# Kernel optimization log

Hardware: AMD Instinct MI355X
Metric: run time of the kernel (lower is better)

Reference implementation:

```python
import jax, jax.numpy as jnp
import numpy as np

NL, D, H, DFF = 6, 1024, 16, 4096
HD = D // H


def _rope(x):
    # x: [B, L, H, HD]; rotate-half RoPE applied along seq dim 1
    L = x.shape[1]
    half = HD // 2
    inv = 1.0 / (10000.0 ** (jnp.arange(half, dtype=jnp.float32) / half))
    ang = jnp.arange(L, dtype=jnp.float32)[:, None] * inv  # [L, half]
    cos = jnp.cos(ang)[None, :, None, :]
    sin = jnp.sin(ang)[None, :, None, :]
    x1, x2 = x[..., :half], x[..., half:]
    return jnp.concatenate([x1 * cos - x2 * sin, x1 * sin + x2 * cos], axis=-1)


def _ln(x, eps=1e-5):
    m = jnp.mean(x, axis=-1, keepdims=True)
    v = jnp.var(x, axis=-1, keepdims=True)
    return (x - m) * jax.lax.rsqrt(v + eps)


def _adaln(x, emb, w, b):
    # emb: [B,1,D] -> squeeze; proj -> gamma,beta
    gb = emb[:, 0, :] @ w.T + b  # [B, 2D]
    g, be = jnp.split(gb, 2, axis=-1)
    return _ln(x) * (1.0 + g[:, None, :]) + be[:, None, :]


def _attn(q, k, v, mask):
    # q:[B,Lq,H,HD] k,v:[B,Lkv,H,HD] mask:[B,Lkv] True=ignore
    scores = jnp.einsum('bqhd,bkhd->bhqk', q, k) / np.float32(np.sqrt(HD))
    scores = jnp.where(mask[:, None, None, :], jnp.float32(-jnp.inf), scores)
    w = jax.nn.softmax(scores, axis=-1)
    return jnp.einsum('bhqk,bkhd->bqhd', w, v)


def setup_inputs() -> dict:
    key = jax.random.key(0)
    ks = jax.random.split(key, 20)
    B, L, LC = 4, 1024, 512
    s = 0.02
    inp = {
        'x': jax.random.normal(ks[0], (B, L, D), jnp.float32),
        'noise_emb': jax.random.normal(ks[1], (B, 1, D), jnp.float32),
        'context': jax.random.normal(ks[2], (B, LC, D), jnp.float32),
        'src_mask': jnp.zeros((B, L), bool),
        'ctx_mask': jnp.zeros((B, LC), bool),
        'n1_w': jax.random.normal(ks[3], (NL, 2 * D, D), jnp.float32) * s,
        'n1_b': jnp.zeros((NL, 2 * D), jnp.float32),
        'n2_w': jax.random.normal(ks[4], (NL, 2 * D, D), jnp.float32) * s,
        'n2_b': jnp.zeros((NL, 2 * D), jnp.float32),
        'n3_w': jax.random.normal(ks[5], (NL, 2 * D, D), jnp.float32) * s,
        'n3_b': jnp.zeros((NL, 2 * D), jnp.float32),
        'qkv_w': jax.random.normal(ks[6], (NL, 3 * D, D), jnp.float32) * s,
        'so_w': jax.random.normal(ks[7], (NL, D, D), jnp.float32) * s,
        'cq_w': jax.random.normal(ks[8], (NL, D, D), jnp.float32) * s,
        'ck_w': jax.random.normal(ks[9], (NL, D, D), jnp.float32) * s,
        'cv_w': jax.random.normal(ks[10], (NL, D, D), jnp.float32) * s,
        'co_w': jax.random.normal(ks[11], (NL, D, D), jnp.float32) * s,
        'f1_w': jax.random.normal(ks[12], (NL, DFF, D), jnp.float32) * s,
        'f1_b': jnp.zeros((NL, DFF), jnp.float32),
        'f2_w': jax.random.normal(ks[13], (NL, D, DFF), jnp.float32) * s,
        'f2_b': jnp.zeros((NL, D), jnp.float32),
    }
    return inp


def reference(x, noise_emb, context, src_mask, ctx_mask,
              n1_w, n1_b, n2_w, n2_b, n3_w, n3_b,
              qkv_w, so_w, cq_w, ck_w, cv_w, co_w,
              f1_w, f1_b, f2_w, f2_b):
    B, L, _ = x.shape
    LC = context.shape[1]
    for i in range(NL):
        # self-attention with AdaLN pre-norm
        xn = _adaln(x, noise_emb, n1_w[i], n1_b[i])
        qkv = xn @ qkv_w[i].T  # [B,L,3D]
        q, k, v = jnp.split(qkv, 3, axis=-1)
        q = _rope(q.reshape(B, L, H, HD))
        k = _rope(k.reshape(B, L, H, HD))
        v = v.reshape(B, L, H, HD)
        a = _attn(q, k, v, src_mask).reshape(B, L, D) @ so_w[i].T
        x = x + a
        # cross-attention with AdaLN pre-norm
        xn = _adaln(x, noise_emb, n2_w[i], n2_b[i])
        q = _rope((xn @ cq_w[i].T).reshape(B, L, H, HD))
        k = _rope((context @ ck_w[i].T).reshape(B, LC, H, HD))
        v = (context @ cv_w[i].T).reshape(B, LC, H, HD)
        a = _attn(q, k, v, ctx_mask).reshape(B, L, D) @ co_w[i].T
        x = x + a
        # FFN with AdaLN pre-norm
        xn = _adaln(x, noise_emb, n3_w[i], n3_b[i])
        h = jax.nn.gelu(xn @ f1_w[i].T + f1_b[i], approximate=False)
        x = x + (h @ f2_w[i].T + f2_b[i])
    return x
```

## Files before the change

### kernel.cpp

```cpp
#include <hip/hip_runtime.h>
#include <hip/hip_bf16.h>
#include <math.h>

#define D_    1024
#define H_    16
#define HD_   64
#define NL_   6
#define DFF_  4096
#define B_    4
#define L_    1024
#define LC_   512

typedef short bf16x8 __attribute__((ext_vector_type(8)));
typedef float f32x4  __attribute__((ext_vector_type(4)));
typedef unsigned int uint32;

__device__ __forceinline__ float waveReduceSum(float v) {
#pragma unroll
  for (int off = 32; off > 0; off >>= 1) v += __shfl_xor(v, off);
  return v;
}
__device__ __forceinline__ ushort f2bf(float f) {
  union { __hip_bfloat16 h; ushort u; } c;
  c.h = __float2bfloat16(f);
  return c.u;
}
__device__ __forceinline__ float bf2f(ushort u) {
  union { uint32 i; float f; } c;
  c.i = ((uint32)u) << 16;
  return c.f;
}
__device__ __forceinline__ uint32 pk2(float a, float b) {
  return (uint32)f2bf(a) | ((uint32)f2bf(b) << 16);
}
__device__ __forceinline__ void gload16(const ushort* g, ushort* l) {
  __builtin_amdgcn_global_load_lds(
      (const __attribute__((address_space(1))) uint32*)g,
      (__attribute__((address_space(3))) uint32*)l, 16, 0, 0);
}

__global__ __launch_bounds__(256) void cvt_bf16_kernel(
    const float* __restrict__ in, ushort* __restrict__ out, int n4) {
  int i = blockIdx.x * 256 + threadIdx.x;
  int stride = gridDim.x * 256;
  for (; i < n4; i += stride) {
    float4 v = ((const float4*)in)[i];
    ushort4 o = {f2bf(v.x), f2bf(v.y), f2bf(v.z), f2bf(v.w)};
    ((ushort4*)out)[i] = o;
  }
}

__global__ __launch_bounds__(256) void cvt_pack_kv_kernel(
    const float* __restrict__ ck, const float* __restrict__ cv,
    ushort* __restrict__ out, int n4) {
  int i = blockIdx.x * 256 + threadIdx.x;
  int stride = gridDim.x * 256;
  for (; i < n4; i += stride) {
    int row = i >> 8;
    int cb = i & 255;
    int layer = row >> 11;
    int sel = (row >> 10) & 1;
    int r = row & 1023;
    const float* src = (sel ? cv : ck) +
                       (((size_t)layer << 10) + r) * 1024 + cb * 4;
    float4 v = *(const float4*)src;
    ushort4 o = {f2bf(v.x), f2bf(v.y), f2bf(v.z), f2bf(v.w)};
    ((ushort4*)out)[i] = o;
  }
}

__global__ void rope_table_kernel(float* __restrict__ tab) {
  int t = blockIdx.x * 256 + threadIdx.x;
  if (t >= L_ * 32) return;
  int l = t >> 5, j = t & 31;
  float inv = powf(10000.f, -(float)j * (1.f / 32.f));
  float ang = (float)l * inv;
  tab[l * 64 + j] = cosf(ang);
  tab[l * 64 + 32 + j] = sinf(ang);
}

__global__ __launch_bounds__(256) void adaln_gb_all_kernel(
    const float* __restrict__ emb,
    const float* __restrict__ n1w, const float* __restrict__ n2w,
    const float* __restrict__ n3w,
    const float* __restrict__ n1b, const float* __restrict__ n2b,
    const float* __restrict__ n3b,
    float* __restrict__ gb) {
  int wid = blockIdx.x * 4 + (threadIdx.x >> 6);
  int lane = threadIdx.x & 63;
  int n = wid & 2047;
  int g = wid >> 11;
  int layer = g / 3, j = g - layer * 3;
  const float* wbase = (j == 0 ? n1w : (j == 1 ? n2w : n3w));
  const float* bbase = (j == 0 ? n1b : (j == 1 ? n2b : n3b));
  const float* wr = wbase + ((size_t)layer * 2048 + n) * 1024;
  float s0 = 0.f, s1 = 0.f, s2 = 0.f, s3 = 0.f;
#pragma unroll
  for (int k4 = 0; k4 < 4; ++k4) {
    int idx = k4 * 64 + lane;
    float4 w4 = ((const float4*)wr)[idx];
    float4 e0 = ((const float4*)emb)[idx];
    float4 e1 = ((const float4*)(emb + 1024))[idx];
    float4 e2 = ((const float4*)(emb + 2048))[idx];
    float4 e3 = ((const float4*)(emb + 3072))[idx];
    s0 += w4.x * e0.x + w4.y * e0.y + w4.z * e0.z + w4.w * e0.w;
    s1 += w4.x * e1.x + w4.y * e1.y + w4.z * e1.z + w4.w * e1.w;
    s2 += w4.x * e2.x + w4.y * e2.y + w4.z * e2.z + w4.w * e2.w;
    s3 += w4.x * e3.x + w4.y * e3.y + w4.z * e3.z + w4.w * e3.w;
  }
  s0 = waveReduceSum(s0);
  s1 = waveReduceSum(s1);
  s2 = waveReduceSum(s2);
  s3 = waveReduceSum(s3);
  if (lane == 0) {
    float bb = bbase[(size_t)layer * 2048 + n];
    gb[((size_t)g * 4 + 0) * 2048 + n] = s0 + bb;
    gb[((size_t)g * 4 + 1) * 2048 + n] = s1 + bb;
    gb[((size_t)g * 4 + 2) * 2048 + n] = s2 + bb;
    gb[((size_t)g * 4 + 3) * 2048 + n] = s3 + bb;
  }
}

__global__ __launch_bounds__(256) void adaln_apply_kernel(
    const float* __restrict__ x, const float* __restrict__ gb,
    ushort* __restrict__ xn) {
  int r = blockIdx.x;
  int b = r >> 10;
  const float* xr = x + (size_t)r * D_;
  int tid = threadIdx.x;
  float4 v = *(const float4*)(xr + tid * 4);
  float s = v.x + v.y + v.z + v.w;
  float q = v.x * v.x + v.y * v.y + v.z * v.z + v.w * v.w;
  s = waveReduceSum(s);
  q = waveReduceSum(q);
  __shared__ float ssum[4], ssq[4], stats[2];
  int w = tid >> 6, lane = tid & 63;
  if (lane == 0) { ssum[w] = s; ssq[w] = q; }
  __syncthreads();
  if (tid == 0) {
    float S = ssum[0] + ssum[1] + ssum[2] + ssum[3];
    float Q = ssq[0] + ssq[1] + ssq[2] + ssq[3];
    float mean = S * (1.f / D_);
    float var = Q * (1.f / D_) - mean * mean;
    stats[0] = mean;
    stats[1] = rsqrtf(var + 1e-5f);
  }
  __syncthreads();
  float mean = stats[0], rstd = stats[1];
  const float* gp = gb + (size_t)b * 2048;
  float4 g  = *(const float4*)(gp + tid * 4);
  float4 be = *(const float4*)(gp + D_ + tid * 4);
  ushort4 o;
  o.x = f2bf((v.x - mean) * rstd * (1.f + g.x) + be.x);
  o.y = f2bf((v.y - mean) * rstd * (1.f + g.y) + be.y);
  o.z = f2bf((v.z - mean) * rstd * (1.f + g.z) + be.z);
  o.w = f2bf((v.w - mean) * rstd * (1.f + g.w) + be.w);
  *(ushort4*)(xn + (size_t)r * D_ + tid * 4) = o;
}

template <int FLAGS, bool OUTBF, int ROPE>
__global__ __launch_bounds__(256) void gemm_mfma_kernel(
    const ushort* __restrict__ A, int lda,
    const ushort* __restrict__ W, int ldw,
    const float* __restrict__ bias,
    const float* __restrict__ res, int ldres,
    void* __restrict__ Cout, int ldc, int K,
    const float* __restrict__ tab, int rlim, int lmask) {
  __shared__ __align__(16) ushort lds[24576];
  const int tid = threadIdx.x;
  const int lane = tid & 63, wv = tid >> 6;
  const int wrow = (wv >> 1) * 64, wcol = (wv & 1) * 64;
  const int fr = lane & 15;
  const int kbs = (((lane >> 4) ^ (fr & 3)) & 3) * 8;

  const int nwg = gridDim.x * gridDim.y;
  const int wg = blockIdx.y * gridDim.x + blockIdx.x;
  const int q = nwg >> 3;
  const int swz = (wg & 7) * q + (wg >> 3);
  const int row0 = (swz / gridDim.x) * 128;
  const int col0 = (swz % gridDim.x) * 128;

  const int c0 = wv * 2, c1 = wv * 2 + 1;
  const int sr = lane >> 2;
  const int sc = (((lane & 3) ^ (sr & 3)) & 3) * 8;
  const ushort* Ap0 = A + (size_t)(row0 + c0 * 16 + sr) * lda + sc;
  const ushort* Ap1 = A + (size_t)(row0 + c1 * 16 + sr) * lda + sc;
  const ushort* Wp0 = W + (size_t)(col0 + c0 * 16 + sr) * ldw + sc;
  const ushort* Wp1 = W + (size_t)(col0 + c1 * 16 + sr) * ldw + sc;

  f32x4 acc[4][4];
#pragma unroll
  for (int m = 0; m < 4; ++m)
#pragma unroll
    for (int n = 0; n < 4; ++n) acc[m][n] = (f32x4)0.f;

#define ASB(B) (lds + (B) * 4096)
#define WSB(B) (lds + 12288 + (B) * 4096)
#define STAGE(B, T)                                   \
  do {                                                \
    const int koff_ = (T) * 32;                       \
    gload16(Ap0 + koff_, ASB(B) + c0 * 512);          \
    gload16(Ap1 + koff_, ASB(B) + c1 * 512);          \
    gload16(Wp0 + koff_, WSB(B) + c0 * 512);          \
    gload16(Wp1 + koff_, WSB(B) + c1 * 512);          \
  } while (0)
#define WAITV8() asm volatile("s_waitcnt vmcnt(8)" ::: "memory")
#define WAITV4() asm volatile("s_waitcnt vmcnt(4)" ::: "memory")
#define WAITV0() asm volatile("s_waitcnt vmcnt(0)" ::: "memory")
#define BAR()    __builtin_amdgcn_s_barrier()
#define COMPUTE(B)                                                          \
  do {                                                                      \
    bf16x8 af[4], bfr[4];                                                   \
    _Pragma("unroll")                                                       \
    for (int m = 0; m < 4; ++m)                                             \
      af[m] = *(const bf16x8*)(ASB(B) + (wrow + m * 16 + fr) * 32 + kbs);   \
    _Pragma("unroll")                                                       \
    for (int n = 0; n < 4; ++n)                                             \
      bfr[n] = *(const bf16x8*)(WSB(B) + (wcol + n * 16 + fr) * 32 + kbs);  \
    _Pragma("unroll")                                                       \
    for (int m = 0; m < 4; ++m)                                             \
      _Pragma("unroll")                                                     \
      for (int n = 0; n < 4; ++n)                                           \
        acc[m][n] = __builtin_amdgcn_mfma_f32_16x16x32_bf16(af[m], bfr[n],  \
                                                            acc[m][n], 0, 0, 0); \
  } while (0)

  const int NT = K >> 5;
  STAGE(0, 0);
  STAGE(1, 1);
  for (int t = 0; t < NT; t += 3) {
    {
      const bool sA = (t + 2) < NT;
      if (sA) STAGE(2, t + 2);
      if ((t + 1) < NT) { if (sA) WAITV8(); else WAITV4(); } else WAITV0();
      BAR(); COMPUTE(0); BAR();
    }
    if ((t + 1) < NT) {
      const bool sB = (t + 3) < NT;
      if (sB) STAGE(0, t + 3);
      if ((t + 2) < NT) { if (sB) WAITV8(); else WAITV4(); } else WAITV0();
      BAR(); COMPUTE(1); BAR();
    }
    if ((t + 2) < NT) {
      const bool sC = (t + 4) < NT;
      if (sC) STAGE(1, t + 4);
      if ((t + 3) < NT) { if (sC) WAITV8(); else WAITV4(); } else WAITV0();
      BAR(); COMPUTE(2); BAR();
    }
  }
#undef STAGE
#undef WAITV8
#undef WAITV4
#undef WAITV0
#undef COMPUTE

  float bn[4];
  if (FLAGS & 1) {
#pragma unroll
    for (int n = 0; n < 4; ++n) bn[n] = bias[col0 + wcol + n * 16 + fr];
  }
#define EPI(v, n)                                                     \
  do {                                                                \
    if (FLAGS & 1) (v) += bn[n];                                      \
    if (FLAGS & 2) (v) = 0.5f * (v) * (1.f + erff((v) * 0.70710678118f)); \
  } while (0)

  if (OUTBF) {
    ushort* Ct = lds;
    ushort* Cg = (ushort*)Cout;
#pragma unroll
    for (int m = 0; m < 4; ++m) {
      int lr0 = wrow + m * 16 + (lane >> 4) * 4;
#pragma unroll
      for (int n = 0; n < 4; ++n) {
        int lc = wcol + n * 16 + fr;
#pragma unroll
        for (int r = 0; r < 4; ++r) {
          float v = acc[m][n][r];
          EPI(v, n);
          Ct[(lr0 + r) * 136 + lc] = f2bf(v);
        }
      }
    }
    __syncthreads();
#pragma unroll
    for (int it = 0; it < 8; ++it) {
      int lr = (tid >> 4) + it * 16;
      int lc = (tid & 15) * 8;
      union { int4 v; ushort us[8]; } vv;
      vv.v = *(const int4*)&Ct[lr * 136 + lc];
      if (ROPE && (col0 + lc) < rlim) {
        union { int4 v; ushort us[8]; } pv;
        pv.v = *(const int4*)&Ct[lr * 136 + (lc ^ 32)];
        int l = (row0 + lr) & lmask;
        int j = lc & 31;
        const float* cb = &tab[l * 64 + j];
        bool lowhalf = (lc & 63) < 32;
#pragma unroll
        for (int e = 0; e < 8; ++e) {
          float cc = cb[e], ss = cb[32 + e];
          float xv = bf2f(vv.us[e]), xp = bf2f(pv.us[e]);
          float o = lowhalf ? (xv * cc - xp * ss) : (xp * ss + xv * cc);
          vv.us[e] = f2bf(o);
        }
      }
      *(int4*)&Cg[(size_t)(row0 + lr) * ldc + col0 + lc] = vv.v;
    }
  } else {
    float* Cf = (float*)lds;
    float* Cg = (float*)Cout;
#pragma unroll
    for (int half = 0; half < 2; ++half) {
      if ((wv >> 1) == half) {
#pragma unroll
        for (int m = 0; m < 4; ++m) {
          int lr0 = m * 16 + (lane >> 4) * 4;
#pragma unroll
          for (int n = 0; n < 4; ++n) {
            int lc = wcol + n * 16 + fr;
#pragma unroll
            for (int r = 0; r < 4; ++r) {
              float v = acc[m][n][r];
              EPI(v, n);
              Cf[(lr0 + r) * 132 + lc] = v;
            }
          }
        }
      }
      __syncthreads();
#pragma unroll
      for (int it = 0; it < 8; ++it) {
        int lr = (tid >> 5) + it * 8;
        int lc = (tid & 31) * 4;
        int grow = row0 + half * 64 + lr;
        float4 v = *(const float4*)&Cf[lr * 132 + lc];
        if (FLAGS & 4) {
          float4 rv = *(const float4*)&res[(size_t)grow * ldres + col0 + lc];
          v.x += rv.x; v.y += rv.y; v.z += rv.z; v.w += rv.w;
        }
        *(float4*)&Cg[(size_t)grow * ldc + col0 + lc] = v;
      }
      __syncthreads();
    }
  }
#undef EPI
#undef ASB
#undef WSB
#undef BAR
}

#define SWZ(row, col) (((row) << 6) + ((col) ^ (((row) & 7) << 3)))
__global__ __launch_bounds__(256) void attn_mfma_kernel(
    const ushort* __restrict__ Q, int ldq,
    const ushort* __restrict__ K, int ldk,
    const ushort* __restrict__ V, int ldv,
    ushort* __restrict__ O, int ldo,
    int Lq, int Lk, float scale) {
  __shared__ __align__(16) ushort Ks[2][64 * 64];
  __shared__ __align__(16) ushort Vt[2][64 * 64];
  __shared__ __align__(16) ushort Os[64 * 64];
  const int tid = threadIdx.x;
  const int lane = tid & 63, w = tid >> 6;
  const int fr = lane & 15, hi = lane >> 4, kb = hi * 8;
  const int b = blockIdx.z, h = blockIdx.y, q0 = blockIdx.x * 64;

  bf16x8 aq[2];
  {
    const ushort* qp = Q + (size_t)(b * Lq + q0 + w * 16 + fr) * ldq + h * 64 + kb;
    union { bf16x8 v; ushort us[8]; } t0, t1;
    t0.v = *(const bf16x8*)qp;
    t1.v = *(const bf16x8*)(qp + 32);
#pragma unroll
    for (int e = 0; e < 8; ++e) {
      t0.us[e] = f2bf(bf2f(t0.us[e]) * scale);
      t1.us[e] = f2bf(bf2f(t1.us[e]) * scale);
    }
    aq[0] = t0.v;
    aq[1] = t1.v;
  }

  const ushort* kbase = K + (size_t)(b * Lk + lane) * ldk + h * 64 + w * 16;
  const ushort* vbase = V + (size_t)(b * Lk + lane) * ldv + h * 64 + w * 16;
  int4 kr0, kr1, vr0, vr1;
#define LOADKV(T)                                          \
  do {                                                     \
    const ushort* kp_ = kbase + (size_t)(T) * 64 * ldk;    \
    kr0 = ((const int4*)kp_)[0];                           \
    kr1 = ((const int4*)kp_)[1];                           \
    const ushort* vp_ = vbase + (size_t)(T) * 64 * ldv;    \
    vr0 = ((const int4*)vp_)[0];                           \
    vr1 = ((const int4*)vp_)[1];                           \
  } while (0)
#define WRITEKV(P)                                                   \
  do {                                                               \
    *(int4*)&Ks[P][SWZ(lane, w * 16)]     = kr0;                     \
    *(int4*)&Ks[P][SWZ(lane, w * 16 + 8)] = kr1;                     \
    union { int4 v; ushort us[8]; } u0_, u1_;                        \
    u0_.v = vr0; u1_.v = vr1;                                        \
    _Pragma("unroll")                                                \
    for (int e = 0; e < 8; ++e) Vt[P][SWZ(w * 16 + e, lane)] = u0_.us[e]; \
    _Pragma("unroll")                                                \
    for (int e = 0; e < 8; ++e) Vt[P][SWZ(w * 16 + 8 + e, lane)] = u1_.us[e]; \
  } while (0)

  f32x4 oacc[4];
#pragma unroll
  for (int n = 0; n < 4; ++n) oacc[n] = (f32x4)0.f;
  float mq = -1e30f, lq = 0.f;
  const int ntiles = Lk >> 6;
  const bool lowhalf = (lane < 32);
  const bool sendSelf = (hi == 1 || hi == 2);

  LOADKV(0);
  WRITEKV(0);
  int p = 0;
  for (int t = 0; t < ntiles; ++t) {
    if (t + 1 < ntiles) LOADKV(t + 1);
    __syncthreads();

    f32x4 sacc[4];
#pragma unroll
    for (int n = 0; n < 4; ++n) sacc[n] = (f32x4)0.f;
    __builtin_amdgcn_s_setprio(1);
#pragma unroll
    for (int s = 0; s < 2; ++s) {
#pragma unroll
      for (int n = 0; n < 4; ++n) {
        bf16x8 ak = *(const bf16x8*)&Ks[p][SWZ(n * 16 + fr, s * 32 + kb)];
        sacc[n] = __builtin_amdgcn_mfma_f32_16x16x32_bf16(ak, aq[s], sacc[n], 0, 0, 0);
      }
    }
    __builtin_amdgcn_s_setprio(0);

    float sm = sacc[0][0];
#pragma unroll
    for (int n = 0; n < 4; ++n)
#pragma unroll
      for (int r = 0; r < 4; ++r) sm = fmaxf(sm, sacc[n][r]);
    sm = fmaxf(sm, __shfl_xor(sm, 16));
    sm = fmaxf(sm, __shfl_xor(sm, 32));
    float mnew = fmaxf(mq, sm);
    float corrq = __expf(mq - mnew);
    mq = mnew;
    float pe[4][4];
    float psum = 0.f;
#pragma unroll
    for (int n = 0; n < 4; ++n)
#pragma unroll
      for (int r = 0; r < 4; ++r) {
        pe[n][r] = __expf(sacc[n][r] - mnew);
        psum += pe[n][r];
      }
    psum += __shfl_xor(psum, 16);
    psum += __shfl_xor(psum, 32);
    lq = lq * corrq + psum;
    float c0 = __shfl(corrq, hi * 4 + 0);
    float c1 = __shfl(corrq, hi * 4 + 1);
    float c2 = __shfl(corrq, hi * 4 + 2);
    float c3 = __shfl(corrq, hi * 4 + 3);
#pragma unroll
    for (int n = 0; n < 4; ++n) {
      oacc[n][0] *= c0; oacc[n][1] *= c1; oacc[n][2] *= c2; oacc[n][3] *= c3;
    }

    uint32 u00 = pk2(pe[0][0], pe[0][1]), u01 = pk2(pe[0][2], pe[0][3]);
    uint32 u10 = pk2(pe[1][0], pe[1][1]), u11 = pk2(pe[1][2], pe[1][3]);
    uint32 u20 = pk2(pe[2][0], pe[2][1]), u21 = pk2(pe[2][2], pe[2][3]);
    uint32 u30 = pk2(pe[3][0], pe[3][1]), u31 = pk2(pe[3][2], pe[3][3]);
    uint32 selfw0 = lowhalf ? u00 : u10;
    uint32 selfw1 = lowhalf ? u01 : u11;
    uint32 selfw2 = lowhalf ? u20 : u30;
    uint32 selfw3 = lowhalf ? u21 : u31;
    uint32 send10 = lowhalf ? u10 : u00;
    uint32 send11 = lowhalf ? u11 : u01;
    uint32 send12 = lowhalf ? u30 : u20;
    uint32 send13 = lowhalf ? u31 : u21;
    uint32 farw0 = __shfl_xor((int)send10, 32);
    uint32 farw1 = __shfl_xor((int)send11, 32);
    uint32 farw2 = __shfl_xor((int)send12, 32);
    uint32 farw3 = __shfl_xor((int)send13, 32);
    uint32 s20 = sendSelf ? selfw0 : farw0;
    uint32 s21 = sendSelf ? selfw1 : farw1;
    uint32 s22 = sendSelf ? selfw2 : farw2;
    uint32 s23 = sendSelf ? selfw3 : farw3;
    uint32 rcv0 = __shfl_xor((int)s20, 16);
    uint32 rcv1 = __shfl_xor((int)s21, 16);
    uint32 rcv2 = __shfl_xor((int)s22, 16);
    uint32 rcv3 = __shfl_xor((int)s23, 16);
    union { uint32 wd[4]; bf16x8 v; } pa0, pa1;
    if (hi == 0) {
      pa0.wd[0] = selfw0; pa0.wd[1] = selfw1; pa0.wd[2] = rcv0; pa0.wd[3] = rcv1;
      pa1.wd[0] = selfw2; pa1.wd[1] = selfw3; pa1.wd[2] = rcv2; pa1.wd[3] = rcv3;
    } else if (hi == 1) {
      pa0.wd[0] = rcv0; pa0.wd[1] = rcv1; pa0.wd[2] = farw0; pa0.wd[3] = farw1;
      pa1.wd[0] = rcv2; pa1.wd[1] = rcv3; pa1.wd[2] = farw2; pa1.wd[3] = farw3;
    } else if (hi == 2) {
      pa0.wd[0] = farw0; pa0.wd[1] = farw1; pa0.wd[2] = rcv0; pa0.wd[3] = rcv1;
      pa1.wd[0] = farw2; pa1.wd[1] = farw3; pa1.wd[2] = rcv2; pa1.wd[3] = rcv3;
    } else {
      pa0.wd[0] = rcv0; pa0.wd[1] = rcv1; pa0.wd[2] = selfw0; pa0.wd[3] = selfw1;
      pa1.wd[0] = rcv2; pa1.wd[1] = rcv3; pa1.wd[2] = selfw2; pa1.wd[3] = selfw3;
    }

    __builtin_amdgcn_s_setprio(1);
#pragma unroll
    for (int n = 0; n < 4; ++n) {
      bf16x8 bv0 = *(const bf16x8*)&Vt[p][SWZ(n * 16 + fr, 0 * 32 + kb)];
      oacc[n] = __builtin_amdgcn_mfma_f32_16x16x32_bf16(pa0.v, bv0, oacc[n], 0, 0, 0);
      bf16x8 bv1 = *(const bf16x8*)&Vt[p][SWZ(n * 16 + fr, 1 * 32 + kb)];
      oacc[n] = __builtin_amdgcn_mfma_f32_16x16x32_bf16(pa1.v, bv1, oacc[n], 0, 0, 0);
    }
    __builtin_amdgcn_s_setprio(0);

    __syncthreads();
    if (t + 1 < ntiles) WRITEKV(p ^ 1);
    p ^= 1;
  }
#undef LOADKV
#undef WRITEKV

  float linv[4];
#pragma unroll
  for (int r = 0; r < 4; ++r) linv[r] = 1.f / __shfl(lq, hi * 4 + r);
#pragma unroll
  for (int r = 0; r < 4; ++r) {
    int rl = w * 16 + hi * 4 + r;
#pragma unroll
    for (int n = 0; n < 4; ++n)
      Os[SWZ(rl, n * 16 + fr)] = f2bf(oacc[n][r] * linv[r]);
  }
  __syncthreads();
  {
    int row = tid >> 2, cbk = (tid & 3) * 16;
    ushort* op = O + (size_t)(b * Lq + q0 + row) * ldo + h * 64 + cbk;
    int4 o0 = *(const int4*)&Os[SWZ(row, cbk)];
    int4 o1 = *(const int4*)&Os[SWZ(row, cbk + 8)];
    ((int4*)op)[0] = o0;
    ((int4*)op)[1] = o1;
  }
}

extern "C" void kernel_launch(void* const* d_in, const int* in_sizes, int n_in,
                              void* d_out, int out_size, void* d_ws, size_t ws_size,
                              hipStream_t stream) {
  const float* x_in = (const float*)d_in[0];
  const float* emb  = (const float*)d_in[1];
  const float* ctx  = (const float*)d_in[2];
  const float* n1w = (const float*)d_in[5];
  const float* n1b = (const float*)d_in[6];
  const float* n2w = (const float*)d_in[7];
  const float* n2b = (const float*)d_in[8];
  const float* n3w = (const float*)d_in[9];
  const float* n3b = (const float*)d_in[10];
  const float* qkvw = (const float*)d_in[11];
  const float* sow  = (const float*)d_in[12];
  const float* cqw  = (const float*)d_in[13];
  const float* ckw  = (const float*)d_in[14];
  const float* cvw  = (const float*)d_in[15];
  const float* cow  = (const float*)d_in[16];
  const float* f1w  = (const float*)d_in[17];
  const float* f1b  = (const float*)d_in[18];
  const float* f2w  = (const float*)d_in[19];
  const float* f2b  = (const float*)d_in[20];

  float* xcur = (float*)d_out;

  ushort* xnb  = (ushort*)d_ws;
  ushort* big  = xnb + (size_t)4096 * 1024;
  ushort* obb  = big + (size_t)4096 * 4096;
  ushort* kvb  = obb + (size_t)4096 * 1024;
  ushort* ctxb = kvb + (size_t)2048 * 2048;
  float*  gball= (float*)(ctxb + (size_t)2048 * 1024);
  float*  tab  = gball + 18 * 4 * 2048;
  ushort* scrW = (ushort*)(tab + 65536);
  const size_t SZ_QKV = (size_t)NL_ * 3072 * 1024;
  const size_t SZ_SQ  = (size_t)NL_ * 1024 * 1024;
  const size_t SZ_F   = (size_t)NL_ * 4096 * 1024;
  ushort* wqkv = scrW + (size_t)4096 * 1024;
  ushort* wso  = wqkv + SZ_QKV;
  ushort* wcq  = wso + SZ_SQ;
  ushort* wkv  = wcq + SZ_SQ;
  ushort* wco  = wkv + 2 * SZ_SQ;
  ushort* wf1  = wco + SZ_SQ;
  ushort* wf2  = wf1 + SZ_F;
  const size_t need_full = (size_t)((char*)(wf2 + SZ_F) - (char*)d_ws);
  const bool wbfull = (ws_size >= need_full);

  hipMemcpyAsync(xcur, x_in, (size_t)B_ * L_ * D_ * sizeof(float),
                 hipMemcpyDeviceToDevice, stream);
  rope_table_kernel<<<128, 256, 0, stream>>>(tab);
  adaln_gb_all_kernel<<<9216, 256, 0, stream>>>(emb, n1w, n2w, n3w,
                                                n1b, n2b, n3b, gball);
  cvt_bf16_kernel<<<1024, 256, 0, stream>>>(ctx, ctxb,
                                            (int)((size_t)2048 * 1024 / 4));

  if (wbfull) {
    cvt_bf16_kernel<<<2048, 256, 0, stream>>>(qkvw, wqkv, (int)(SZ_QKV / 4));
    cvt_bf16_kernel<<<2048, 256, 0, stream>>>(sow,  wso,  (int)(SZ_SQ / 4));
    cvt_bf16_kernel<<<2048, 256, 0, stream>>>(cqw,  wcq,  (int)(SZ_SQ / 4));
    cvt_pack_kv_kernel<<<2048, 256, 0, stream>>>(ckw, cvw, wkv,
                                                 (int)(2 * SZ_SQ / 4));
    cvt_bf16_kernel<<<2048, 256, 0, stream>>>(cow,  wco,  (int)(SZ_SQ / 4));
    cvt_bf16_kernel<<<2048, 256, 0, stream>>>(f1w,  wf1,  (int)(SZ_F / 4));
    cvt_bf16_kernel<<<2048, 256, 0, stream>>>(f2w,  wf2,  (int)(SZ_F / 4));
  }

  auto prepW = [&](const float* src, ushort* full, size_t layerOff,
                   size_t nelem) -> const ushort* {
    if (wbfull) return full + layerOff;
    cvt_bf16_kernel<<<1024, 256, 0, stream>>>(src + layerOff, scrW,
                                              (int)(nelem / 4));
    return scrW;
  };

  const int ROWS = B_ * L_;
  const dim3 blk(256);

  for (int i = 0; i < NL_; ++i) {
    const float* f1bi = f1b + (size_t)i * DFF_;
    const float* f2bi = f2b + (size_t)i * D_;

    adaln_apply_kernel<<<ROWS, blk, 0, stream>>>(
        xcur, gball + (size_t)(i * 3 + 0) * 4 * 2048, xnb);
    gemm_mfma_kernel<0, true, 1><<<dim3(24, 32), blk, 0, stream>>>(
        xnb, D_, prepW(qkvw, wqkv, (size_t)i * 3072 * 1024, (size_t)3072 * 1024),
        D_, nullptr, nullptr, 0, big, 3072, D_, tab, 2048, 1023);
    attn_mfma_kernel<<<dim3(L_ / 64, H_, B_), blk, 0, stream>>>(
        big, 3072, big + 1024, 3072, big + 2048, 3072, obb, D_, L_, L_, 0.125f);
    gemm_mfma_kernel<4, false, 0><<<dim3(8, 32), blk, 0, stream>>>(
        obb, D_, prepW(sow, wso, (size_t)i * 1024 * 1024, (size_t)1024 * 1024),
        D_, nullptr, xcur, D_, xcur, D_, D_, tab, 0, 0);

    adaln_apply_kernel<<<ROWS, blk, 0, stream>>>(
        xcur, gball + (size_t)(i * 3 + 1) * 4 * 2048, xnb);
    gemm_mfma_kernel<0, true, 1><<<dim3(8, 32), blk, 0, stream>>>(
        xnb, D_, prepW(cqw, wcq, (size_t)i * 1024 * 1024, (size_t)1024 * 1024),
        D_, nullptr, nullptr, 0, big, 1024, D_, tab, 1024, 1023);
    {
      const ushort* wkvi;
      if (wbfull) {
        wkvi = wkv + (size_t)i * 2048 * 1024;
      } else {
        cvt_bf16_kernel<<<512, 256, 0, stream>>>(
            ckw + (size_t)i * 1024 * 1024, scrW, (int)((size_t)1024 * 1024 / 4));
        cvt_bf16_kernel<<<512, 256, 0, stream>>>(
            cvw + (size_t)i * 1024 * 1024, scrW + (size_t)1024 * 1024,
            (int)((size_t)1024 * 1024 / 4));
        wkvi = scrW;
      }
      gemm_mfma_kernel<0, true, 1><<<dim3(16, 16), blk, 0, stream>>>(
          ctxb, D_, wkvi, D_, nullptr, nullptr, 0, kvb, 2048, D_, tab, 1024, 511);
    }
    attn_mfma_kernel<<<dim3(L_ / 64, H_, B_), blk, 0, stream>>>(
        big, 1024, kvb, 2048, kvb + 1024, 2048, obb, D_, L_, LC_, 0.125f);
    gemm_mfma_kernel<4, false, 0><<<dim3(8, 32), blk, 0, stream>>>(
        obb, D_, prepW(cow, wco, (size_t)i * 1024 * 1024, (size_t)1024 * 1024),
        D_, nullptr, xcur, D_, xcur, D_, D_, tab, 0, 0);

    adaln_apply_kernel<<<ROWS, blk, 0, stream>>>(
        xcur, gball + (size_t)(i * 3 + 2) * 4 * 2048, xnb);
    gemm_mfma_kernel<3, true, 0><<<dim3(32, 32), blk, 0, stream>>>(
        xnb, D_, prepW(f1w, wf1, (size_t)i * 4096 * 1024, (size_t)4096 * 1024),
        D_, f1bi, nullptr, 0, big, DFF_, D_, tab, 0, 0);
    gemm_mfma_kernel<5, false, 0><<<dim3(8, 32), blk, 0, stream>>>(
        big, DFF_, prepW(f2w, wf2, (size_t)i * 4096 * 1024, (size_t)4096 * 1024),
        DFF_, f2bi, xcur, D_, xcur, D_, DFF_, tab, 0, 0);
  }
}
```

Before: 2.167 ms.

## Add 256x256-tile 512-thread GEMM kernel for QKV and FFN1 projections

Introduces a new bf16 MFMA GEMM kernel with 256x256 output tiles, 8 waves per workgroup, double-buffered 64-wide K stages in 128KB LDS, XOR-swizzled LDS layout, and a workgroup-index swizzle for L2 locality. It replaces the older GEMM for the QKV projection (with fused RoPE epilogue) and the FFN up-projection (bias+GELU epilogue). The larger tiles raise arithmetic intensity and cut redundant global loads. The cost is fewer workgroups (192/256) on a GPU with many CUs, plus higher register and LDS pressure that may limit occupancy.

```diff
diff --git a/kernel.cpp b/kernel.cpp
--- a/kernel.cpp
+++ b/kernel.cpp
@@ -347,6 +347,139 @@
 #undef ASB
 #undef WSB
 #undef BAR
+}
+
+template <int FLAGS, int ROPE>
+__global__ __launch_bounds__(512, 2) void gemm256_kernel(
+    const ushort* __restrict__ A, int lda,
+    const ushort* __restrict__ W, int ldw,
+    const float* __restrict__ bias,
+    ushort* __restrict__ Cout, int ldc, int K,
+    const float* __restrict__ tab, int rlim, int lmask) {
+  __shared__ __align__(16) ushort lds[65536];
+  const int tid = threadIdx.x;
+  const int lane = tid & 63, wid = tid >> 6;
+  const int wm = wid >> 2, wn = wid & 3;
+  const int fr = lane & 15, hi = lane >> 4;
+
+  const int nwg = gridDim.x * gridDim.y;
+  const int wg = blockIdx.y * gridDim.x + blockIdx.x;
+  const int q = nwg >> 3;
+  const int swz = (wg & 7) * q + (wg >> 3);
+  const int row0 = (swz / gridDim.x) * 256;
+  const int col0 = (swz % gridDim.x) * 256;
+
+  const int srow = lane >> 3;
+  const int scol = ((lane & 7) ^ srow) * 8;
+  const ushort* Asrc[4];
+  const ushort* Wsrc[4];
+#pragma unroll
+  for (int j = 0; j < 4; ++j) {
+    int r = wid * 32 + j * 8 + srow;
+    Asrc[j] = A + (size_t)(row0 + r) * lda + scol;
+    Wsrc[j] = W + (size_t)(col0 + r) * ldw + scol;
+  }
+#define AB256(b) (lds + (b) * 16384)
+#define WB256(b) (lds + 32768 + (b) * 16384)
+#define STG256(b, T)                                      \
+  do {                                                    \
+    const int kk_ = (T) * 64;                             \
+    _Pragma("unroll")                                     \
+    for (int j = 0; j < 4; ++j) {                         \
+      int ch_ = wid * 4 + j;                              \
+      gload16(Asrc[j] + kk_, AB256(b) + ch_ * 512);       \
+      gload16(Wsrc[j] + kk_, WB256(b) + ch_ * 512);       \
+    }                                                     \
+  } while (0)
+
+  f32x4 acc[8][4];
+#pragma unroll
+  for (int m = 0; m < 8; ++m)
+#pragma unroll
+    for (int n = 0; n < 4; ++n) acc[m][n] = (f32x4)0.f;
+
+  const int NT = K >> 6;
+  STG256(0, 0);
+  asm volatile("s_waitcnt vmcnt(0)" ::: "memory");
+  __builtin_amdgcn_s_barrier();
+  for (int t = 0; t < NT; ++t) {
+    const int cur = t & 1;
+    if (t + 1 < NT) STG256(cur ^ 1, t + 1);
+    const ushort* ab = AB256(cur);
+    const ushort* wb = WB256(cur);
+    __builtin_amdgcn_s_setprio(1);
+#pragma unroll
+    for (int s = 0; s < 2; ++s) {
+      bf16x8 wf[4];
+#pragma unroll
+      for (int n = 0; n < 4; ++n) {
+        int row = wn * 64 + n * 16 + fr;
+        wf[n] = *(const bf16x8*)(wb + row * 64 + (((s * 4 + hi) ^ (fr & 7)) * 8));
+      }
+#pragma unroll
+      for (int m = 0; m < 8; ++m) {
+        int row = wm * 128 + m * 16 + fr;
+        bf16x8 af = *(const bf16x8*)(ab + row * 64 + (((s * 4 + hi) ^ (fr & 7)) * 8));
+#pragma unroll
+        for (int n = 0; n < 4; ++n)
+          acc[m][n] = __builtin_amdgcn_mfma_f32_16x16x32_bf16(af, wf[n],
+                                                              acc[m][n], 0, 0, 0);
+      }
+    }
+    __builtin_amdgcn_s_setprio(0);
+    asm volatile("s_waitcnt vmcnt(0)" ::: "memory");
+    __builtin_amdgcn_s_barrier();
+  }
+#undef STG256
+
+  float bn[4];
+  if (FLAGS & 1) {
+#pragma unroll
+    for (int n = 0; n < 4; ++n) bn[n] = bias[col0 + wn * 64 + n * 16 + fr];
+  }
+  ushort* Ct = lds;
+#pragma unroll
+  for (int m = 0; m < 8; ++m) {
+    int lr0 = wm * 128 + m * 16 + hi * 4;
+#pragma unroll
+    for (int n = 0; n < 4; ++n) {
+      int lc = wn * 64 + n * 16 + fr;
+#pragma unroll
+      for (int r = 0; r < 4; ++r) {
+        float v = acc[m][n][r];
+        if (FLAGS & 1) v += bn[n];
+        if (FLAGS & 2) v = 0.5f * v * (1.f + erff(v * 0.70710678118f));
+        Ct[(lr0 + r) * 256 + lc] = f2bf(v);
+      }
+    }
+  }
+  __syncthreads();
+#pragma unroll
+  for (int it = 0; it < 16; ++it) {
+    int idx = tid + it * 512;
+    int lr = idx >> 5;
+    int lc = (idx & 31) * 8;
+    union { int4 v; ushort us[8]; } vv;
+    vv.v = *(const int4*)&Ct[lr * 256 + lc];
+    if (ROPE && (col0 + lc) < rlim) {
+      union { int4 v; ushort us[8]; } pv;
+      pv.v = *(const int4*)&Ct[lr * 256 + (lc ^ 32)];
+      int l = (row0 + lr) & lmask;
+      int j = lc & 31;
+      const float* cb = &tab[l * 64 + j];
+      bool lowhalf = (lc & 63) < 32;
+#pragma unroll
+      for (int e = 0; e < 8; ++e) {
+        float cc = cb[e], ss = cb[32 + e];
+        float xv = bf2f(vv.us[e]), xp = bf2f(pv.us[e]);
+        float o = lowhalf ? (xv * cc - xp * ss) : (xp * ss + xv * cc);
+        vv.us[e] = f2bf(o);
+      }
+    }
+    *(int4*)&Cout[(size_t)(row0 + lr) * ldc + col0 + lc] = vv.v;
+  }
+#undef AB256
+#undef WB256
 }
 
 #define SWZ(row, col) (((row) << 6) + ((col) ^ (((row) & 7) << 3)))
@@ -615,6 +748,7 @@
 
   const int ROWS = B_ * L_;
   const dim3 blk(256);
+  const dim3 blk512(512);
 
   for (int i = 0; i < NL_; ++i) {
     const float* f1bi = f1b + (size_t)i * DFF_;
@@ -622,9 +756,9 @@
 
     adaln_apply_kernel<<<ROWS, blk, 0, stream>>>(
         xcur, gball + (size_t)(i * 3 + 0) * 4 * 2048, xnb);
-    gemm_mfma_kernel<0, true, 1><<<dim3(24, 32), blk, 0, stream>>>(
+    gemm256_kernel<0, 1><<<dim3(12, 16), blk512, 0, stream>>>(
         xnb, D_, prepW(qkvw, wqkv, (size_t)i * 3072 * 1024, (size_t)3072 * 1024),
-        D_, nullptr, nullptr, 0, big, 3072, D_, tab, 2048, 1023);
+        D_, nullptr, big, 3072, D_, tab, 2048, 1023);
     attn_mfma_kernel<<<dim3(L_ / 64, H_, B_), blk, 0, stream>>>(
         big, 3072, big + 1024, 3072, big + 2048, 3072, obb, D_, L_, L_, 0.125f);
     gemm_mfma_kernel<4, false, 0><<<dim3(8, 32), blk, 0, stream>>>(
@@ -659,9 +793,9 @@
 
     adaln_apply_kernel<<<ROWS, blk, 0, stream>>>(
         xcur, gball + (size_t)(i * 3 + 2) * 4 * 2048, xnb);
-    gemm_mfma_kernel<3, true, 0><<<dim3(32, 32), blk, 0, stream>>>(
+    gemm256_kernel<3, 0><<<dim3(16, 16), blk512, 0, stream>>>(
         xnb, D_, prepW(f1w, wf1, (size_t)i * 4096 * 1024, (size_t)4096 * 1024),
-        D_, f1bi, nullptr, 0, big, DFF_, D_, tab, 0, 0);
+        D_, f1bi, big, DFF_, D_, tab, 0, 0);
     gemm_mfma_kernel<5, false, 0><<<dim3(8, 32), blk, 0, stream>>>(
         big, DFF_, prepW(f2w, wf2, (size_t)i * 4096 * 1024, (size_t)4096 * 1024),
         DFF_, f2bi, xcur, D_, xcur, D_, DFF_, tab, 0, 0);
```

New measurement: 2.164 ms. No clear change (-0.2%).
